# Kernel tuning notes

Hardware: AMD Instinct MI355X
Metric: run time of the kernel (lower is better)

## Reference

```python
import jax, jax.numpy as jnp
import numpy as np

N_TERMS = 2048  # zonotope error terms (x[0] center + 2047 generators)
N = 4096        # neurons


def setup_inputs() -> dict:
    key = jax.random.key(0)
    x = jax.random.normal(key, (N_TERMS, N), dtype=jnp.float32)
    return {"x": x}


def reference(x):
    n_terms, n = x.shape
    # interval bounds of the zonotope
    abs_sum = jnp.sum(jnp.abs(x[1:]), axis=0)      # [n]
    upper = x[0] + abs_sum
    lower = x[0] - abs_sum

    cross = (lower * upper) < 0                    # neuron straddles 0
    pos = lower >= 0                               # strictly non-negative
    crossf = cross.astype(x.dtype)
    posf = pos.astype(x.dtype)

    # 'auto' lambda init: upper/(upper-lower) on crossing neurons, 1 on positive,
    # NaN (0/0) replaced by 0.5; lambda is set via .data => constant w.r.t. x.
    denom = upper - lower
    safe = denom != 0
    lam = posf + crossf * jnp.where(safe, upper / jnp.where(safe, denom, 1.0), 0.5)
    lam = jax.lax.stop_gradient(lam)

    delta = jnp.maximum(-lam * lower, (1.0 - lam) * upper)  # [n]

    center = (delta * 0.5 + lam * x[0]) * crossf + x[0] * posf
    gens = x[1:] * (lam * crossf + posf)                    # [n_terms-1, n]

    # Parallel stream-compaction: crossing neuron i gets its own new error row
    # at n_terms + (# crossings before i). Padded to worst case n new rows;
    # non-crossing writes land on distinct (row, col) slots with value 0.
    ci = cross.astype(jnp.int32)
    rows = n_terms + jnp.cumsum(ci) - ci               # exclusive prefix sum
    cols = jnp.arange(n)

    out = jnp.zeros((n_terms + n, n), x.dtype)
    out = out.at[0].set(center)
    out = out.at[1:n_terms].set(gens)
    out = out.at[rows, cols].add((delta * 0.5) * crossf)
    return out
```

## Files before the change

### kernel.cpp

```cpp
#include <hip/hip_runtime.h>

#define N_TERMS 2048
#define NCOL 4096
#define NC4 1024
#define NCHUNK 128
#define RPC (N_TERMS / NCHUNK)

typedef float f4_t __attribute__((ext_vector_type(4)));

__global__ void k_partial_abs(const float* __restrict__ x, float* __restrict__ partial) {
    int col4 = blockIdx.x * blockDim.x + threadIdx.x;
    int chunk = blockIdx.y;
    int r0 = chunk * RPC;
    int r1 = r0 + RPC;
    if (r0 == 0) r0 = 1;
    const f4_t* x4 = (const f4_t*)x;
    f4_t acc = {0.f, 0.f, 0.f, 0.f};
#pragma unroll
    for (int r = r0; r < r1; ++r) {
        f4_t v = x4[(long)r * NC4 + col4];
        acc.x += fabsf(v.x);
        acc.y += fabsf(v.y);
        acc.z += fabsf(v.z);
        acc.w += fabsf(v.w);
    }
    ((f4_t*)partial)[chunk * NC4 + col4] = acc;
}

__global__ void k_stats(const float* __restrict__ x, const float* __restrict__ partial,
                        float* __restrict__ out0, float* __restrict__ scale,
                        float* __restrict__ dhalf, int* __restrict__ crossflag) {
    const int t = threadIdx.x;
    const int lane = t & 63;
    const int q = t >> 6;
    const int c = blockIdx.x * 64 + lane;

    float s0 = 0.f, s1 = 0.f, s2 = 0.f, s3 = 0.f;
    const int k0 = q * 32;
#pragma unroll 8
    for (int k = 0; k < 32; k += 4) {
        s0 += partial[(k0 + k + 0) * NCOL + c];
        s1 += partial[(k0 + k + 1) * NCOL + c];
        s2 += partial[(k0 + k + 2) * NCOL + c];
        s3 += partial[(k0 + k + 3) * NCOL + c];
    }
    __shared__ float red[4][64];
    red[q][lane] = (s0 + s1) + (s2 + s3);
    __syncthreads();
    if (q == 0) {
        float s = (red[0][lane] + red[1][lane]) + (red[2][lane] + red[3][lane]);
        float x0 = x[c];
        float u = x0 + s;
        float l = x0 - s;
        bool cross = (l * u) < 0.0f;
        bool pos = (l >= 0.0f);
        float denom = u - l;
        float lam = (pos ? 1.0f : 0.0f) +
                    (cross ? ((denom != 0.0f) ? u / denom : 0.5f) : 0.0f);
        float delta = fmaxf(-lam * l, (1.0f - lam) * u);
        float crossf = cross ? 1.0f : 0.0f;
        float posf = pos ? 1.0f : 0.0f;
        out0[c] = (delta * 0.5f + lam * x0) * crossf + x0 * posf;
        scale[c] = lam * crossf + posf;
        dhalf[c] = delta * 0.5f * crossf;
        crossflag[c] = cross ? 1 : 0;
    }
}

__global__ void k_prefix(const int* __restrict__ crossflag, int* __restrict__ rowtarget) {
    const int T = 256;
    const int PER = NCOL / T;
    __shared__ int tsum[T];
    int t = threadIdx.x;
    int base = t * PER;
    int ex[PER];
    int run = 0;
#pragma unroll
    for (int i = 0; i < PER; ++i) {
        ex[i] = run;
        run += crossflag[base + i];
    }
    tsum[t] = run;
    __syncthreads();
    for (int off = 1; off < T; off <<= 1) {
        int v = 0;
        if (t >= off) v = tsum[t - off];
        __syncthreads();
        tsum[t] += v;
        __syncthreads();
    }
    int excl = (t == 0) ? 0 : tsum[t - 1];
#pragma unroll
    for (int i = 0; i < PER; ++i) rowtarget[base + i] = N_TERMS + excl + ex[i];
}

__global__ void k_write(const float* __restrict__ x, const float* __restrict__ scale,
                        const float* __restrict__ dhalf, const int* __restrict__ rowtarget,
                        float* __restrict__ out) {
    long g = (long)blockIdx.x * blockDim.x + threadIdx.x;
    int col4 = (int)(g & 1023);
    int group = (int)(g >> 10);
    int r0 = group << 2;
    const f4_t* x4 = (const f4_t*)x;
    f4_t* o4 = (f4_t*)out;

    if (group < 512) {
        f4_t sc = ((const f4_t*)scale)[col4];
        if (group == 0) {
#pragma unroll
            for (int r = 1; r < 4; ++r) {
                f4_t v = x4[(long)r * NC4 + col4] * sc;
                __builtin_nontemporal_store(v, &o4[(long)r * NC4 + col4]);
            }
        } else {
#pragma unroll
            for (int i = 0; i < 4; ++i) {
                int r = r0 + i;
                f4_t v = x4[(long)r * NC4 + col4] * sc;
                __builtin_nontemporal_store(v, &o4[(long)r * NC4 + col4]);
            }
        }
    } else {
        int4 rt = ((const int4*)rowtarget)[col4];
        f4_t dh = ((const f4_t*)dhalf)[col4];
#pragma unroll
        for (int i = 0; i < 4; ++i) {
            int r = r0 + i;
            f4_t v;
            v.x = (rt.x == r) ? dh.x : 0.0f;
            v.y = (rt.y == r) ? dh.y : 0.0f;
            v.z = (rt.z == r) ? dh.z : 0.0f;
            v.w = (rt.w == r) ? dh.w : 0.0f;
            __builtin_nontemporal_store(v, &o4[(long)r * NC4 + col4]);
        }
    }
}

extern "C" void kernel_launch(void* const* d_in, const int* in_sizes, int n_in,
                              void* d_out, int out_size, void* d_ws, size_t ws_size,
                              hipStream_t stream) {
    const float* x = (const float*)d_in[0];
    float* out = (float*)d_out;

    float* ws = (float*)d_ws;
    float* partial   = ws;
    float* scale     = partial + NCHUNK * NCOL;
    float* dhalf     = scale + NCOL;
    int*   crossflag = (int*)(dhalf + NCOL);
    int*   rowtarget = crossflag + NCOL;

    k_partial_abs<<<dim3(NC4 / 256, NCHUNK), 256, 0, stream>>>(x, partial);
    k_stats<<<64, 256, 0, stream>>>(x, partial, out, scale, dhalf, crossflag);
    k_prefix<<<1, 256, 0, stream>>>(crossflag, rowtarget);

    const int blocks = 1536 * 1024 / 256;
    k_write<<<blocks, 256, 0, stream>>>(x, scale, dhalf, rowtarget, out);
}
```

Measured before the change: 138.5 us.

## Fuse all four stages into one cooperative kernel with grid syncs

Replaces the four separate launches (partial abs-sum, stats, prefix scan, write) with a single cooperative kernel of 512 blocks that separates the phases with grid-wide syncs. The scaled-generator copy now runs right after the prefix scan without waiting on a grid sync, and the write phases become grid-stride loops over rows. This removes per-launch overhead and inter-kernel gaps. In exchange, grid syncs cost time, only 512 resident blocks do the bandwidth-bound copy, and most blocks sit idle during the stats and scan phases.

```diff
diff --git a/kernel.cpp b/kernel.cpp
--- a/kernel.cpp
+++ b/kernel.cpp
@@ -1,131 +1,133 @@
 #include <hip/hip_runtime.h>
+#include <hip/hip_cooperative_groups.h>
+
+namespace cg = cooperative_groups;
 
 #define N_TERMS 2048
 #define NCOL 4096
 #define NC4 1024
 #define NCHUNK 128
 #define RPC (N_TERMS / NCHUNK)
+#define NBLK 512
+#define NTHR 256
 
 typedef float f4_t __attribute__((ext_vector_type(4)));
 
-__global__ void k_partial_abs(const float* __restrict__ x, float* __restrict__ partial) {
-    int col4 = blockIdx.x * blockDim.x + threadIdx.x;
-    int chunk = blockIdx.y;
-    int r0 = chunk * RPC;
-    int r1 = r0 + RPC;
-    if (r0 == 0) r0 = 1;
-    const f4_t* x4 = (const f4_t*)x;
-    f4_t acc = {0.f, 0.f, 0.f, 0.f};
-#pragma unroll
-    for (int r = r0; r < r1; ++r) {
-        f4_t v = x4[(long)r * NC4 + col4];
-        acc.x += fabsf(v.x);
-        acc.y += fabsf(v.y);
-        acc.z += fabsf(v.z);
-        acc.w += fabsf(v.w);
-    }
-    ((f4_t*)partial)[chunk * NC4 + col4] = acc;
-}
-
-__global__ void k_stats(const float* __restrict__ x, const float* __restrict__ partial,
-                        float* __restrict__ out0, float* __restrict__ scale,
-                        float* __restrict__ dhalf, int* __restrict__ crossflag) {
+__global__ __launch_bounds__(NTHR, 2) void k_fused(
+    const float* __restrict__ x, float* __restrict__ out,
+    float* __restrict__ partial, float* __restrict__ scale,
+    float* __restrict__ dhalf, int* __restrict__ crossflag,
+    int* __restrict__ rowtarget)
+{
+    cg::grid_group gg = cg::this_grid();
     const int t = threadIdx.x;
-    const int lane = t & 63;
-    const int q = t >> 6;
-    const int c = blockIdx.x * 64 + lane;
-
-    float s0 = 0.f, s1 = 0.f, s2 = 0.f, s3 = 0.f;
-    const int k0 = q * 32;
-#pragma unroll 8
-    for (int k = 0; k < 32; k += 4) {
-        s0 += partial[(k0 + k + 0) * NCOL + c];
-        s1 += partial[(k0 + k + 1) * NCOL + c];
-        s2 += partial[(k0 + k + 2) * NCOL + c];
-        s3 += partial[(k0 + k + 3) * NCOL + c];
-    }
-    __shared__ float red[4][64];
-    red[q][lane] = (s0 + s1) + (s2 + s3);
-    __syncthreads();
-    if (q == 0) {
-        float s = (red[0][lane] + red[1][lane]) + (red[2][lane] + red[3][lane]);
-        float x0 = x[c];
-        float u = x0 + s;
-        float l = x0 - s;
-        bool cross = (l * u) < 0.0f;
-        bool pos = (l >= 0.0f);
-        float denom = u - l;
-        float lam = (pos ? 1.0f : 0.0f) +
-                    (cross ? ((denom != 0.0f) ? u / denom : 0.5f) : 0.0f);
-        float delta = fmaxf(-lam * l, (1.0f - lam) * u);
-        float crossf = cross ? 1.0f : 0.0f;
-        float posf = pos ? 1.0f : 0.0f;
-        out0[c] = (delta * 0.5f + lam * x0) * crossf + x0 * posf;
-        scale[c] = lam * crossf + posf;
-        dhalf[c] = delta * 0.5f * crossf;
-        crossflag[c] = cross ? 1 : 0;
-    }
-}
-
-__global__ void k_prefix(const int* __restrict__ crossflag, int* __restrict__ rowtarget) {
-    const int T = 256;
-    const int PER = NCOL / T;
-    __shared__ int tsum[T];
-    int t = threadIdx.x;
-    int base = t * PER;
-    int ex[PER];
-    int run = 0;
-#pragma unroll
-    for (int i = 0; i < PER; ++i) {
-        ex[i] = run;
-        run += crossflag[base + i];
-    }
-    tsum[t] = run;
-    __syncthreads();
-    for (int off = 1; off < T; off <<= 1) {
-        int v = 0;
-        if (t >= off) v = tsum[t - off];
-        __syncthreads();
-        tsum[t] += v;
-        __syncthreads();
-    }
-    int excl = (t == 0) ? 0 : tsum[t - 1];
-#pragma unroll
-    for (int i = 0; i < PER; ++i) rowtarget[base + i] = N_TERMS + excl + ex[i];
-}
-
-__global__ void k_write(const float* __restrict__ x, const float* __restrict__ scale,
-                        const float* __restrict__ dhalf, const int* __restrict__ rowtarget,
-                        float* __restrict__ out) {
-    long g = (long)blockIdx.x * blockDim.x + threadIdx.x;
-    int col4 = (int)(g & 1023);
-    int group = (int)(g >> 10);
-    int r0 = group << 2;
+    const int b = blockIdx.x;
     const f4_t* x4 = (const f4_t*)x;
     f4_t* o4 = (f4_t*)out;
 
-    if (group < 512) {
-        f4_t sc = ((const f4_t*)scale)[col4];
-        if (group == 0) {
+    __shared__ float red[4][64];
+    __shared__ int tsum[NTHR];
+
+    {
+        const int col4 = (b & 3) * NTHR + t;
+        const int chunk = b >> 2;
+        int r0 = chunk * RPC;
+        const int r1 = r0 + RPC;
+        if (r0 == 0) r0 = 1;
+        f4_t acc = {0.f, 0.f, 0.f, 0.f};
+        for (int r = r0; r < r1; ++r) {
+            f4_t v = x4[(long)r * NC4 + col4];
+            acc.x += fabsf(v.x);
+            acc.y += fabsf(v.y);
+            acc.z += fabsf(v.z);
+            acc.w += fabsf(v.w);
+        }
+        ((f4_t*)partial)[chunk * NC4 + col4] = acc;
+    }
+    gg.sync();
+
+    if (b < 64) {
+        const int lane = t & 63;
+        const int q = t >> 6;
+        const int c = b * 64 + lane;
+
+        float s0 = 0.f, s1 = 0.f, s2 = 0.f, s3 = 0.f;
+        const int k0 = q * 32;
+#pragma unroll 8
+        for (int k = 0; k < 32; k += 4) {
+            s0 += partial[(k0 + k + 0) * NCOL + c];
+            s1 += partial[(k0 + k + 1) * NCOL + c];
+            s2 += partial[(k0 + k + 2) * NCOL + c];
+            s3 += partial[(k0 + k + 3) * NCOL + c];
+        }
+        red[q][lane] = (s0 + s1) + (s2 + s3);
+        __syncthreads();
+        if (q == 0) {
+            float s = (red[0][lane] + red[1][lane]) + (red[2][lane] + red[3][lane]);
+            float x0 = x[c];
+            float u = x0 + s;
+            float l = x0 - s;
+            bool cross = (l * u) < 0.0f;
+            bool pos = (l >= 0.0f);
+            float denom = u - l;
+            float lam = (pos ? 1.0f : 0.0f) +
+                        (cross ? ((denom != 0.0f) ? u / denom : 0.5f) : 0.0f);
+            float delta = fmaxf(-lam * l, (1.0f - lam) * u);
+            float crossf = cross ? 1.0f : 0.0f;
+            float posf = pos ? 1.0f : 0.0f;
+            out[c] = (delta * 0.5f + lam * x0) * crossf + x0 * posf;
+            scale[c] = lam * crossf + posf;
+            dhalf[c] = delta * 0.5f * crossf;
+            crossflag[c] = cross ? 1 : 0;
+        }
+    }
+    gg.sync();
+
+    if (b == 0) {
+        const int PER = NCOL / NTHR;
+        const int base = t * PER;
+        int ex[16];
+        int run = 0;
 #pragma unroll
-            for (int r = 1; r < 4; ++r) {
-                f4_t v = x4[(long)r * NC4 + col4] * sc;
-                __builtin_nontemporal_store(v, &o4[(long)r * NC4 + col4]);
-            }
-        } else {
+        for (int i = 0; i < PER; ++i) {
+            ex[i] = run;
+            run += crossflag[base + i];
+        }
+        tsum[t] = run;
+        __syncthreads();
+        for (int off = 1; off < NTHR; off <<= 1) {
+            int v = 0;
+            if (t >= off) v = tsum[t - off];
+            __syncthreads();
+            tsum[t] += v;
+            __syncthreads();
+        }
+        int excl = (t == 0) ? 0 : tsum[t - 1];
 #pragma unroll
-            for (int i = 0; i < 4; ++i) {
-                int r = r0 + i;
-                f4_t v = x4[(long)r * NC4 + col4] * sc;
-                __builtin_nontemporal_store(v, &o4[(long)r * NC4 + col4]);
-            }
+        for (int i = 0; i < PER; ++i) rowtarget[base + i] = N_TERMS + excl + ex[i];
+    }
+
+    {
+        const int g = b * NTHR + t;
+        const int col4 = g & 1023;
+        const int rstart = 1 + (g >> 10);
+        const f4_t sc = ((const f4_t*)scale)[col4];
+#pragma unroll 4
+        for (int r = rstart; r < N_TERMS; r += 128) {
+            f4_t v = x4[(long)r * NC4 + col4];
+            __builtin_nontemporal_store(v * sc, &o4[(long)r * NC4 + col4]);
         }
-    } else {
-        int4 rt = ((const int4*)rowtarget)[col4];
-        f4_t dh = ((const f4_t*)dhalf)[col4];
-#pragma unroll
-        for (int i = 0; i < 4; ++i) {
-            int r = r0 + i;
+    }
+    gg.sync();
+
+    {
+        const int g = b * NTHR + t;
+        const int col4 = g & 1023;
+        const int rstart = N_TERMS + (g >> 10);
+        const int4 rt = ((const int4*)rowtarget)[col4];
+        const f4_t dh = ((const f4_t*)dhalf)[col4];
+#pragma unroll 4
+        for (int r = rstart; r < N_TERMS + NCOL; r += 128) {
             f4_t v;
             v.x = (rt.x == r) ? dh.x : 0.0f;
             v.y = (rt.y == r) ? dh.y : 0.0f;
@@ -149,10 +151,8 @@
     int*   crossflag = (int*)(dhalf + NCOL);
     int*   rowtarget = crossflag + NCOL;
 
-    k_partial_abs<<<dim3(NC4 / 256, NCHUNK), 256, 0, stream>>>(x, partial);
-    k_stats<<<64, 256, 0, stream>>>(x, partial, out, scale, dhalf, crossflag);
-    k_prefix<<<1, 256, 0, stream>>>(crossflag, rowtarget);
-
-    const int blocks = 1536 * 1024 / 256;
-    k_write<<<blocks, 256, 0, stream>>>(x, scale, dhalf, rowtarget, out);
+    void* args[] = {(void*)&x, (void*)&out, (void*)&partial, (void*)&scale,
+                    (void*)&dhalf, (void*)&crossflag, (void*)&rowtarget};
+    hipLaunchCooperativeKernel((void*)k_fused, dim3(NBLK), dim3(NTHR),
+                               args, 0, stream);
 }
```

Result: slower. 319.1 us (+130.5%).
